# Kernel tuning notes

Hardware: AMD Instinct MI355X
Metric: run time of the kernel (lower is better)

## Reference

```python
import jax, jax.numpy as jnp
import numpy as np

SIGMA = 0.002  # TreeEnergyLoss default; edge weight = exp(-||df||^2 / sigma)


def bilinear_resize(x, oh, ow):
    """F.interpolate(mode='bilinear', align_corners=False), no antialias. x: [B,C,H,W]."""
    B, C, H, W = x.shape
    if (H, W) == (oh, ow):
        return x
    def coords(o, n):
        s = (jnp.arange(o, dtype=jnp.float32) + 0.5) * (n / o) - 0.5
        s = jnp.clip(s, 0.0, n - 1.0)
        lo = jnp.floor(s).astype(jnp.int32)
        hi = jnp.minimum(lo + 1, n - 1)
        return lo, hi, s - lo.astype(jnp.float32)
    r0, r1, rf = coords(oh, H)
    c0, c1, cf = coords(ow, W)
    xr = x[:, :, r0, :] * (1.0 - rf)[None, None, :, None] + x[:, :, r1, :] * rf[None, None, :, None]
    return xr[:, :, :, c0] * (1.0 - cf) + xr[:, :, :, c1] * cf


def nearest_resize(x, oh, ow):
    B, C, H, W = x.shape
    if (H, W) == (oh, ow):
        return x
    ri = jnp.floor(jnp.arange(oh) * (H / oh)).astype(jnp.int32)
    ci = jnp.floor(jnp.arange(ow) * (W / ow)).astype(jnp.int32)
    return x[:, :, ri, :][:, :, :, ci]


def _mst_bfs_np(embed, H, W):
    """Kruskal MST on the 4-connected pixel grid (edge cost = squared L2 feature
    distance, as in MinimumSpanningTree(TreeFilter2D.norm2_distance)), then BFS
    order from vertex 0. embed: np [C,H,W]. Returns (sorted_index, sorted_parent)
    where sorted_parent is the BFS position of each vertex's parent."""
    V = H * W
    idx = np.arange(V).reshape(H, W)
    eu = np.concatenate([idx[:-1, :].ravel(), idx[:, :-1].ravel()])
    ev = np.concatenate([idx[1:, :].ravel(), idx[:, 1:].ravel()])
    f = embed.reshape(embed.shape[0], V)
    cost = ((f[:, eu] - f[:, ev]) ** 2).sum(0)
    parent = np.arange(V)
    def find(x):
        root = x
        while parent[root] != root:
            root = parent[root]
        while parent[x] != root:
            parent[x], x = root, parent[x]
        return root
    nbr = [[] for _ in range(V)]
    cnt = 0
    for e in np.argsort(cost, kind='stable'):
        u, v = int(eu[e]), int(ev[e])
        ru, rv = find(u), find(v)
        if ru != rv:
            parent[ru] = rv
            nbr[u].append(v)
            nbr[v].append(u)
            cnt += 1
            if cnt == V - 1:
                break
    sorted_index = np.empty(V, np.int32)
    sorted_parent = np.empty(V, np.int32)
    visited = np.zeros(V, bool)
    sorted_index[0] = 0; sorted_parent[0] = 0; visited[0] = True
    head, tail = 0, 1
    while head < tail:
        u = int(sorted_index[head])
        for v in nbr[u]:
            if not visited[v]:
                visited[v] = True
                sorted_index[tail] = v
                sorted_parent[tail] = head
                tail += 1
        head += 1
    return sorted_index, sorted_parent


def build_trees(embed):
    """embed: [B,C,H,W]. Host-side MST+BFS per batch element (torch.no_grad in original)."""
    e = np.asarray(jax.lax.stop_gradient(embed), dtype=np.float64)
    B, C, H, W = e.shape
    si, sp = zip(*[_mst_bfs_np(e[b], H, W) for b in range(B)])
    return jnp.asarray(np.stack(si)), jnp.asarray(np.stack(sp))


def _tree_filter_single(f, embed, sorted_index, sorted_parent):
    """Normalized tree filter: out_i = sum_j W_ij f_j / sum_j W_ij with
    W_ij = prod of exp(-||de||^2/sigma) along the unique tree path i->j.
    Computed exactly via bottom-up aggregation + top-down propagation in BFS order.
    f: [C,V], embed: [Ce,V]."""
    C, V = f.shape
    fs = f[:, sorted_index]                        # [C,V] features in BFS order
    es = embed[:, sorted_index]
    d = ((es - es[:, sorted_parent]) ** 2).sum(0)  # [V]; d[0]=0 (root self edge)
    w = jnp.exp(-d / SIGMA)                        # edge weight to parent
    # bottom-up: children have larger BFS index, so reverse order is valid.
    # extra ones-row carries the normalizer Z through the same recursion.
    S0 = jnp.concatenate([fs, jnp.ones((1, V), fs.dtype)], axis=0)
    def up(S, j):
        return S.at[:, sorted_parent[j]].add(w[j] * S[:, j]), None
    S, _ = jax.lax.scan(up, S0, jnp.arange(V - 1, 0, -1))
    # top-down: A_root = S_root; A_j = S_j + w_j * (A_parent - w_j * S_j)
    def down(A, j):
        p = sorted_parent[j]
        return A.at[:, j].set(S[:, j] + w[j] * (A[:, p] - w[j] * S[:, j])), None
    A0 = jnp.zeros_like(S).at[:, 0].set(S[:, 0])
    A, _ = jax.lax.scan(down, A0, jnp.arange(1, V))
    out_sorted = A[:C] / A[C]
    return jnp.zeros_like(f).at[:, sorted_index].set(out_sorted)


def tree_filter(feature, embed, si, sp):
    B, C, h, w = feature.shape
    out = jax.vmap(_tree_filter_single)(
        feature.reshape(B, C, h * w),
        embed.reshape(B, embed.shape[1], h * w), si, sp)
    return out.reshape(B, C, h, w)


def setup_inputs():
    key = jax.random.key(0)
    k1, k2, k3, k4 = jax.random.split(key, 4)
    preds = jax.random.normal(k1, (8, 21, 80, 80), jnp.float32)
    # scaled so exp(-||df||^2 / 0.002) gives non-degenerate edge weights
    low_feats = jax.random.uniform(k2, (8, 3, 80, 80), jnp.float32) * 0.02
    high_feats = jax.random.normal(k3, (8, 256, 80, 80), jnp.float32) * 0.002
    unlabeled_ROIs = jax.random.randint(k4, (8, 80, 80), 0, 2, dtype=jnp.int32)
    return {"preds": preds, "low_feats": low_feats,
            "high_feats": high_feats, "unlabeled_ROIs": unlabeled_ROIs}


def reference(preds, low_feats, high_feats, unlabeled_ROIs):
    B, C, h, w = preds.shape
    low = bilinear_resize(low_feats, h, w)  # under torch.no_grad in original
    roi = nearest_resize(unlabeled_ROIs[:, None].astype(jnp.float32), h, w)
    si_l, sp_l = build_trees(low)
    si_h, sp_h = build_trees(high_feats)
    prob = jax.nn.softmax(preds, axis=1)
    AS = tree_filter(prob, jax.lax.stop_gradient(low), si_l, sp_l)  # low-level tree
    AS = tree_filter(AS, high_feats, si_h, sp_h)                    # high-level tree
    N = roi.sum()
    loss = (roi * jnp.abs(prob - AS)).sum()
    return jnp.where(N > 0, loss / N, jnp.zeros((), preds.dtype))  # weight = 1.0
```

## Files before the change

### kernel.cpp

```cpp
#include <hip/hip_runtime.h>

#define BB 8
#define CP 21
#define CF 22
#define CLOW 3
#define CHIGH 256
#define WW 80
#define VV 6400
#define EVERT 6320
#define EE 12640
#define TT 16
#define SIGMA_F 0.002f
#define ROOT 3240

#define NE (VV - 1)
#define NA (2 * NE)
#define NILA 0xFFFFu
#define NB 200

__device__ __forceinline__ void edge_uv(int e, int& u, int& v) {
  if (e < EVERT) { u = e; v = e + WW; }
  else { int e2 = e - EVERT; int r = e2 / (WW - 1); int c = e2 - r * (WW - 1); u = r * WW + c; v = u + 1; }
}

__global__ void k_softmax(const float* __restrict__ preds, float* __restrict__ prob) {
  int i = blockIdx.x * blockDim.x + threadIdx.x;
  if (i >= BB * VV) return;
  int b = i / VV, v = i - b * VV;
  const float* p = preds + (size_t)b * CP * VV + v;
  float m = -1e30f;
  #pragma unroll
  for (int c = 0; c < CP; c++) m = fmaxf(m, p[c * VV]);
  float e[CP], s = 0.f;
  #pragma unroll
  for (int c = 0; c < CP; c++) { float x = expf(p[c * VV] - m); e[c] = x; s += x; }
  float inv = 1.f / s;
  float* o = prob + (size_t)b * CP * VV + v;
  #pragma unroll
  for (int c = 0; c < CP; c++) o[c * VV] = e[c] * inv;
}

__global__ void k_edgekey(const float* __restrict__ low, const float* __restrict__ high,
                          unsigned long long* __restrict__ ekey) {
  int i = blockIdx.x * blockDim.x + threadIdx.x;
  if (i >= TT * EE) return;
  int t = i / EE, e = i - t * EE;
  int u, v; edge_uv(e, u, v);
  double acc = 0.0;
  if (t < BB) {
    const float* emb = low + (size_t)t * CLOW * VV;
    for (int c = 0; c < CLOW; c++) { double d = (double)emb[c * VV + u] - (double)emb[c * VV + v]; acc += d * d; }
  } else {
    const float* emb = high + (size_t)(t - BB) * CHIGH * VV;
    for (int c = 0; c < CHIGH; c++) { double d = (double)emb[c * VV + u] - (double)emb[c * VV + v]; acc += d * d; }
  }
  unsigned long long bits = (unsigned long long)__double_as_longlong(acc);
  ekey[i] = (bits & ~0x3FFFULL) | (unsigned long long)e;
}

__global__ __launch_bounds__(1024) void k_boruvka(const unsigned long long* __restrict__ ekey,
    int* __restrict__ mstU, int* __restrict__ mstV) {
  int t = blockIdx.x;
  const unsigned long long* key = ekey + (size_t)t * EE;
  int* mu = mstU + t * VV;
  int* mv = mstV + t * VV;
  __shared__ int comp[VV];
  __shared__ unsigned long long bst[VV];
  __shared__ unsigned short tgtS[VV];
  __shared__ unsigned short el0[EE];
  __shared__ unsigned short el1[EE];
  __shared__ int changed, cnt, necnt;
  int tid = threadIdx.x;
  const int nt = 1024;
  for (int v = tid; v < VV; v += nt) comp[v] = v;
  for (int e = tid; e < EE; e += nt) el0[e] = (unsigned short)e;
  if (tid == 0) cnt = 0;
  __syncthreads();
  unsigned short* els = el0;
  unsigned short* eld = el1;
  int ecnt = EE;
  for (int round = 0; round < 48 && ecnt > 0; round++) {
    for (int v = tid; v < VV; v += nt) bst[v] = ~0ULL;
    if (tid == 0) { changed = 0; necnt = 0; }
    __syncthreads();
    for (int j = tid; j < ecnt; j += nt) {
      int e = els[j];
      int u, v; edge_uv(e, u, v);
      int cu = comp[u], cv = comp[v];
      if (cu != cv) { unsigned long long k = key[e]; atomicMin(&bst[cu], k); atomicMin(&bst[cv], k); }
    }
    __syncthreads();
    for (int c = tid; c < VV; c += nt) {
      unsigned short tg = (unsigned short)NILA;
      if (comp[c] == c) {
        unsigned long long k = bst[c];
        if (k != ~0ULL) {
          int e = (int)(k & 0x3FFFULL);
          int u, v; edge_uv(e, u, v);
          int cu = comp[u], cv = comp[v];
          tg = (unsigned short)((cu == c) ? cv : cu);
        }
      }
      tgtS[c] = tg;
    }
    __syncthreads();
    for (int c = tid; c < VV; c += nt) {
      int o = tgtS[c];
      if (o == (int)NILA) continue;
      unsigned long long k = bst[c];
      if (bst[o] == k && c < o) continue;
      comp[c] = o;
      int slot = atomicAdd(&cnt, 1);
      int e = (int)(k & 0x3FFFULL);
      int u, v; edge_uv(e, u, v);
      mu[slot] = u; mv[slot] = v;
      changed = 1;
    }
    __syncthreads();
    if (!changed) break;
    for (int v = tid; v < VV; v += nt) {
      int c = comp[v];
      int c2 = comp[c];
      if (c2 != c) {
        int r0 = c2;
        while (true) { int n = comp[r0]; if (n == r0) break; r0 = n; }
        comp[v] = r0;
      }
    }
    __syncthreads();
    for (int j = tid; j < ecnt; j += nt) {
      int e = els[j];
      int u, v; edge_uv(e, u, v);
      if (comp[u] != comp[v]) { int s = atomicAdd(&necnt, 1); eld[s] = (unsigned short)e; }
    }
    __syncthreads();
    ecnt = necnt;
    __syncthreads();
    unsigned short* tp = els; els = eld; eld = tp;
  }
}

__global__ __launch_bounds__(1024) void k_buildtree(const int* __restrict__ mstU, const int* __restrict__ mstV,
    int* __restrict__ ordG, int* __restrict__ spG, int* __restrict__ pvG,
    int* __restrict__ lpG, int* __restrict__ nlevG) {
  int t = blockIdx.x;
  const int* mu = mstU + t * VV;
  const int* mv = mstV + t * VV;
  int tid = threadIdx.x;
  const int nt = 1024;
  int lane = tid & 63, wid = tid >> 6;

  __shared__ int buf4[32004];
  char* buf = (char*)buf4;
  __shared__ int part[64];
  __shared__ short tbl[8 * NB];
  __shared__ unsigned short dbuf2[VV];
  __shared__ int lasts, spackU, spackW, scenter, smaxd;

  int* deg = (int*)(buf + 0);
  int* off = (int*)(buf + 25600);
  unsigned short* adjA = (unsigned short*)(buf + 51208);
  unsigned short* succ = (unsigned short*)(buf + 102408);
  int* pk0 = (int*)(buf + 0);
  int* pk1 = (int*)(buf + 51208);
  unsigned short* r_a = (unsigned short*)(buf + 102408);
  short* H = (short*)(buf + 51208);
  unsigned short* depthR = (unsigned short*)(buf + 76808);
  unsigned short* firstK = (unsigned short*)(buf + 89608);
  short* prefmin = (short*)(buf + 0);
  short* sufmin  = (short*)(buf + 25600);
  unsigned short* distU = (unsigned short*)(buf + 76808);
  unsigned short* parentS = (unsigned short*)(buf + 76808);
  int* lev = (int*)(buf + 0);
  int* cur = (int*)(buf + 25604);
  unsigned short* ordS = (unsigned short*)(buf + 51208);
  unsigned short* posS = (unsigned short*)(buf + 64008);

  auto blockScanEx = [&](int s) -> int {
    int x = s;
    #pragma unroll
    for (int d = 1; d < 64; d <<= 1) { int o = __shfl_up(x, d); if (lane >= d) x += o; }
    if (lane == 63) part[wid] = x;
    __syncthreads();
    if (wid == 0) {
      int y = (lane < 16) ? part[lane] : 0;
      #pragma unroll
      for (int d = 1; d < 16; d <<= 1) { int o = __shfl_up(y, d); if (lane >= d) y += o; }
      if (lane < 16) part[lane] = y;
    }
    __syncthreads();
    int base = (wid > 0) ? part[wid - 1] : 0;
    return base + (x - s);
  };

  for (int v = tid; v < VV; v += nt) deg[v] = 0;
  __syncthreads();
  for (int e = tid; e < NE; e += nt) { atomicAdd(&deg[mu[e]], 1); atomicAdd(&deg[mv[e]], 1); }
  __syncthreads();
  {
    const int SCH = 7;
    int base = tid * SCH;
    int s = 0;
    #pragma unroll
    for (int k = 0; k < SCH; k++) { int v = base + k; if (v < VV) s += deg[v]; }
    int ex = blockScanEx(s);
    #pragma unroll
    for (int k = 0; k < SCH; k++) { int v = base + k; if (v < VV) { off[v] = ex; ex += deg[v]; } }
    if (tid == 1023) off[VV] = ex;
  }
  __syncthreads();
  for (int v = tid; v < VV; v += nt) deg[v] = off[v];
  __syncthreads();
  for (int e = tid; e < NE; e += nt) {
    int u = mu[e], v = mv[e];
    adjA[atomicAdd(&deg[u], 1)] = (unsigned short)(2 * e);
    adjA[atomicAdd(&deg[v], 1)] = (unsigned short)(2 * e + 1);
  }
  __syncthreads();
  for (int v = tid; v < VV; v += nt) {
    int b0 = off[v], dv = off[v + 1] - b0;
    for (int k = 0; k < dv; k++) {
      unsigned short a = adjA[b0 + k];
      unsigned short b = adjA[b0 + ((k + 1 == dv) ? 0 : k + 1)];
      succ[a ^ 1] = b;
    }
  }
  if (tid == 0) lasts = adjA[off[ROOT] + (off[ROOT + 1] - off[ROOT]) - 1] ^ 1;
  __syncthreads();
  if (tid == 0) succ[lasts] = (unsigned short)NILA;
  __syncthreads();
  for (int a = tid; a < NA; a += nt) {
    unsigned int n = succ[a];
    pk0[a] = ((n == NILA ? 0 : 1) << 16) | (int)n;
  }
  __syncthreads();
  {
    int* px = pk0;
    int* py = pk1;
    for (int rd = 0; rd < 14; rd++) {
      for (int a = tid; a < NA; a += nt) {
        int cur_ = px[a];
        int n = cur_ & 0xFFFF;
        if (n != (int)NILA) {
          int o = px[n];
          cur_ = (((cur_ >> 16) + (o >> 16)) << 16) | (o & 0xFFFF);
        }
        py[a] = cur_;
      }
      __syncthreads();
      int* tp = px; px = py; py = tp;
    }
    for (int a = tid; a < NA; a += nt) r_a[a] = (unsigned short)(pk0[a] >> 16);
  }
  __syncthreads();
  for (int a = tid; a < NA; a += nt) {
    int pa = NA - 1 - (int)r_a[a];
    int pb = NA - 1 - (int)r_a[a ^ 1];
    H[pa] = (pa < pb) ? (short)1 : (short)-1;
  }
  __syncthreads();
  {
    const int SCH = 13;
    int base = tid * SCH;
    int lim = base + SCH; if (lim > NA) lim = NA;
    int s = 0;
    for (int j = base; j < lim; j++) s += H[j];
    int run = blockScanEx(s);
    for (int j = base; j < lim; j++) { run += H[j]; H[j] = (short)run; }
  }
  __syncthreads();
  if (tid == 0) { spackU = 0; smaxd = 0; scenter = 0x7FFFFFFF; }
  __syncthreads();
  for (int a = tid; a < NA; a += nt) {
    int pa = NA - 1 - (int)r_a[a];
    int pb = NA - 1 - (int)r_a[a ^ 1];
    if (pa < pb) {
      int e = a >> 1;
      int head = (a & 1) ? mu[e] : mv[e];
      depthR[head] = (unsigned short)H[pa];
      firstK[head] = (unsigned short)(pa + 1);
    }
  }
  if (tid == 0) { depthR[ROOT] = 0; firstK[ROOT] = 0; }
  __syncthreads();
  {
    int loc = 0;
    for (int v = tid; v < VV; v += nt) { int p = ((int)depthR[v] << 13) | v; if (p > loc) loc = p; }
    #pragma unroll
    for (int d = 32; d > 0; d >>= 1) { int o = __shfl_down(loc, d); if (o > loc) loc = o; }
    if (lane == 0) atomicMax(&spackU, loc);
  }
  __syncthreads();
  {
    for (int seg = wid; seg < NB; seg += 16) {
      int p = seg * 64 + lane;
      int h = (p < NA) ? (int)H[p] : 32767;
      int hp = h;
      #pragma unroll
      for (int d = 1; d < 64; d <<= 1) { int o = __shfl_up(hp, d); if (lane >= d && o < hp) hp = o; }
      prefmin[p] = (short)hp;
      int hs = h;
      #pragma unroll
      for (int d = 1; d < 64; d <<= 1) { int o = __shfl_down(hs, d); if (lane + d < 64 && o < hs) hs = o; }
      sufmin[p] = (short)hs;
      if (lane == 0) tbl[seg] = (short)hs;
    }
  }
  __syncthreads();
  for (int k = 1; k < 8; k++) {
    short vv_ = 0;
    if (tid < NB) {
      int o = tid + (1 << (k - 1));
      short a = tbl[(k - 1) * NB + tid];
      short b2 = (o < NB) ? tbl[(k - 1) * NB + o] : (short)32767;
      vv_ = (a < b2) ? a : b2;
    }
    __syncthreads();
    if (tid < NB) tbl[k * NB + tid] = vv_;
    __syncthreads();
  }
  auto distq = [&](int K1, int K2) -> int {
    if (K1 == K2) return 0;
    int l = (K1 < K2 ? K1 : K2) - 1;
    int r = (K1 > K2 ? K1 : K2) - 1;
    int m = 32767;
    int l0 = l < 0 ? 0 : l;
    int bl = l0 >> 6, br = r >> 6;
    if (bl == br) {
      for (int p = l0; p <= r; p++) { int h = H[p]; if (h < m) m = h; }
    } else {
      int a = sufmin[l0], b2 = prefmin[r];
      m = a < b2 ? a : b2;
      int lo = bl + 1, hi = br - 1;
      if (lo <= hi) {
        int L = hi - lo + 1;
        int k = 31 - __builtin_clz(L);
        int c1 = tbl[k * NB + lo];
        int c2 = tbl[k * NB + hi - (1 << k) + 1];
        if (c1 < m) m = c1;
        if (c2 < m) m = c2;
      }
    }
    if (l < 0 && 0 < m) m = 0;
    int h1 = (K1 == 0) ? 0 : (int)H[K1 - 1];
    int h2 = (K2 == 0) ? 0 : (int)H[K2 - 1];
    return h1 + h2 - 2 * m;
  };
  int u = spackU & 0x1FFF;
  int Ku = firstK[u];
  if (tid == 0) spackW = 0;
  __syncthreads();
  {
    int loc = 0;
    for (int v = tid; v < VV; v += nt) {
      int d = distq(Ku, firstK[v]);
      distU[v] = (unsigned short)d;
      int p = (d << 13) | v;
      if (p > loc) loc = p;
    }
    #pragma unroll
    for (int d = 32; d > 0; d >>= 1) { int o = __shfl_down(loc, d); if (o > loc) loc = o; }
    if (lane == 0) atomicMax(&spackW, loc);
  }
  __syncthreads();
  int D = spackW >> 13;
  int w = spackW & 0x1FFF;
  int Kw = firstK[w];
  for (int v = tid; v < VV; v += nt) dbuf2[v] = (unsigned short)distq(Kw, firstK[v]);
  __syncthreads();
  {
    int half = D >> 1;
    for (int v = tid; v < VV; v += nt) {
      if ((int)distU[v] == half && (int)distU[v] + (int)dbuf2[v] == D) atomicMin(&scenter, v);
    }
  }
  __syncthreads();
  int cvert = (scenter == 0x7FFFFFFF) ? ROOT : scenter;
  int Kc = firstK[cvert];
  __syncthreads();
  {
    int loc = 0;
    for (int v = tid; v < VV; v += nt) {
      int d = distq(Kc, firstK[v]);
      dbuf2[v] = (unsigned short)d;
      if (d > loc) loc = d;
    }
    #pragma unroll
    for (int d = 32; d > 0; d >>= 1) { int o = __shfl_down(loc, d); if (o > loc) loc = o; }
    if (lane == 0) atomicMax(&smaxd, loc);
  }
  __syncthreads();
  int maxd = smaxd;
  int sTil = Kc;
  for (int a = tid; a < NA; a += nt) {
    int pa = NA - 1 - (int)r_a[a];
    int pb = NA - 1 - (int)r_a[a ^ 1];
    int pa2 = pa - sTil; if (pa2 < 0) pa2 += NA;
    int pb2 = pb - sTil; if (pb2 < 0) pb2 += NA;
    if (pa2 < pb2) {
      int e = a >> 1;
      int head = (a & 1) ? mu[e] : mv[e];
      int tail = (a & 1) ? mv[e] : mu[e];
      parentS[head] = (unsigned short)tail;
    }
  }
  if (tid == 0) parentS[cvert] = (unsigned short)cvert;
  __syncthreads();
  for (int d = tid; d <= VV; d += nt) lev[d] = 0;
  __syncthreads();
  for (int v = tid; v < VV; v += nt) atomicAdd(&lev[dbuf2[v]], 1);
  __syncthreads();
  {
    const int SCH = 7;
    int base = tid * SCH;
    int s = 0;
    #pragma unroll
    for (int k = 0; k < SCH; k++) { int d = base + k; if (d <= VV) s += lev[d]; }
    int ex = blockScanEx(s);
    #pragma unroll
    for (int k = 0; k < SCH; k++) {
      int d = base + k;
      if (d <= VV) {
        int st = ex;
        ex += lev[d];
        if (d < VV) cur[d] = st;
        lpG[t * (VV + 1) + d] = st;
      }
    }
  }
  __syncthreads();
  for (int v = tid; v < VV; v += nt) {
    int d = dbuf2[v];
    int slot = atomicAdd(&cur[d], 1);
    ordS[slot] = (unsigned short)v;
    posS[v] = (unsigned short)slot;
  }
  __syncthreads();
  for (int j = tid; j < VV; j += nt) {
    int v = ordS[j];
    int pv = parentS[v];
    ordG[t * VV + j] = v;
    pvG[t * VV + j] = pv;
    spG[t * VV + j] = posS[pv];
  }
  if (tid == 0) nlevG[t] = maxd + 1;
}

__global__ void k_weights(const unsigned long long* __restrict__ ekey,
                          const int* __restrict__ ordG, const int* __restrict__ pvG,
                          float* __restrict__ wvp) {
  int i = blockIdx.x * blockDim.x + threadIdx.x;
  if (i >= TT * VV) return;
  int t = i / VV;
  int v = ordG[i], p = pvG[i];
  float wout;
  if (v == p) {
    wout = 1.0f;
  } else {
    int a = v < p ? v : p;
    int diff = v < p ? p - v : v - p;
    int e;
    if (diff == WW) e = a;
    else { int r = a / WW, c = a - r * WW; e = EVERT + r * (WW - 1) + c; }
    unsigned long long k = ekey[(size_t)t * EE + e];
    double cost = __longlong_as_double((long long)(k & ~0x3FFFULL));
    wout = expf(-(float)cost / SIGMA_F);
  }
  wvp[i] = wout;
}

__global__ __launch_bounds__(512) void k_filter_pc(const float* __restrict__ Fsrc, float* __restrict__ Araw,
    const float* __restrict__ wvp, const int* __restrict__ ordG, const int* __restrict__ spG,
    const int* __restrict__ lpG, const int* __restrict__ nlevG, int treeBase) {
  int blk = blockIdx.x;
  int b = blk / CF, ch = blk - b * CF;
  int t = treeBase + b;
  __shared__ alignas(16) char arena[140816];
  float2* ab0 = (float2*)(arena);
  float2* ab1 = (float2*)(arena + 51200);
  float*  S   = (float*)(arena + 51200);
  float*  w   = (float*)(arena + 76800);
  unsigned short* sp0 = (unsigned short*)(arena + 102400);
  unsigned short* sp1 = (unsigned short*)(arena + 115200);
  unsigned short* lpS = (unsigned short*)(arena + 128000);
  const int* ord = ordG + t * VV;
  const int* spt = spG + t * VV;
  const float* wsrc = wvp + t * VV;
  const int* lp = lpG + t * (VV + 1);
  int tid = threadIdx.x;
  const int nt = 512;
  int NL = nlevG[t];
  for (int j = tid; j <= NL; j += nt) lpS[j] = (unsigned short)lp[j];
  const bool norm_in = (treeBase != 0);
  for (int j = tid; j < VV; j += nt) {
    sp0[j] = (unsigned short)spt[j];
    w[j] = wsrc[j];
    float val;
    if (ch < CP) {
      int v = ord[j];
      if (!norm_in) val = Fsrc[((size_t)b * CP + ch) * VV + v];
      else          val = Fsrc[((size_t)b * CF + ch) * VV + v] / Fsrc[((size_t)b * CF + CP) * VV + v];
    } else val = 1.0f;
    S[j] = val;
  }
  __syncthreads();
  if (tid < 64) {
    int s1 = lpS[NL];
    int s0 = lpS[NL - 1];
    for (int l = NL - 1; l >= 1; l--) {
      int s0n = (l > 1) ? (int)lpS[l - 1] : 0;
      for (int j = s0 + tid; j < s1; j += 64) {
        atomicAdd(&S[sp0[j]], w[j] * S[j]);
      }
      asm volatile("s_waitcnt lgkmcnt(0)" ::: "memory");
      __builtin_amdgcn_sched_barrier(0);
      s1 = s0; s0 = s0n;
    }
  }
  __syncthreads();
  for (int j = tid; j < VV; j += nt) {
    float wv = w[j];
    float a = (j == 0) ? 0.f : wv;
    float bv = (j == 0) ? S[0] : S[j] * (1.f - wv * wv);
    ab0[j] = make_float2(a, bv);
  }
  __syncthreads();
  int rounds = 0;
  { int d = 1; while (d < NL) { d <<= 1; rounds++; } }
  float2 *abs_ = ab0, *abd_ = ab1;
  unsigned short *ps_ = sp0, *pd_ = sp1;
  for (int r = 0; r < rounds; r++) {
    for (int j = tid; j < VV; j += nt) {
      float2 m = abs_[j];
      int p = ps_[j];
      float2 o = m;
      int pn = p;
      if (m.x != 0.f) {
        float2 mp = abs_[p];
        pn = ps_[p];
        o.x = m.x * mp.x;
        o.y = fmaf(m.x, mp.y, m.y);
      }
      abd_[j] = o;
      pd_[j] = (unsigned short)pn;
    }
    __syncthreads();
    float2* tf = abs_; abs_ = abd_; abd_ = tf;
    unsigned short* tu = ps_; ps_ = pd_; pd_ = tu;
  }
  float* Ob = Araw + ((size_t)b * CF + ch) * VV;
  for (int j = tid; j < VV; j += nt) Ob[ord[j]] = abs_[j].y;
}

__global__ void k_loss(const float* __restrict__ prob, const float* __restrict__ Araw2,
                       const int* __restrict__ roi, double* __restrict__ acc) {
  int i = blockIdx.x * blockDim.x + threadIdx.x;
  int tid = threadIdx.x;
  double s = 0.0, n = 0.0;
  if (i < BB * VV) {
    int b = i / VV, v = i - b * VV;
    if (roi[i] != 0) {
      n = 1.0;
      const float* pb = prob + (size_t)b * CP * VV + v;
      const float* ab = Araw2 + (size_t)b * CF * VV + v;
      float inv = 1.0f / ab[CP * VV];
      float ls = 0.f;
      #pragma unroll
      for (int c = 0; c < CP; c++) ls += fabsf(pb[c * VV] - ab[c * VV] * inv);
      s = (double)ls;
    }
  }
  __shared__ double rs[256], rn[256];
  rs[tid] = s; rn[tid] = n;
  __syncthreads();
  for (int d = 128; d > 0; d >>= 1) {
    if (tid < d) { rs[tid] += rs[tid + d]; rn[tid] += rn[tid + d]; }
    __syncthreads();
  }
  if (tid == 0) { atomicAdd(&acc[0], rs[0]); atomicAdd(&acc[1], rn[0]); }
}

__global__ void k_finalize(const double* __restrict__ acc, float* __restrict__ out) {
  out[0] = (acc[1] > 0.0) ? (float)(acc[0] / acc[1]) : 0.0f;
}

extern "C" void kernel_launch(void* const* d_in, const int* in_sizes, int n_in,
                              void* d_out, int out_size, void* d_ws, size_t ws_size,
                              hipStream_t stream) {
  const float* preds = (const float*)d_in[0];
  const float* low   = (const float*)d_in[1];
  const float* high  = (const float*)d_in[2];
  const int*   roi   = (const int*)d_in[3];
  float* out = (float*)d_out;

  char* w = (char*)d_ws;
  size_t off = 0;
  auto alloc = [&](size_t bytes) -> void* {
    void* p = w + off;
    off += (bytes + 255) & ~(size_t)255;
    return p;
  };
  float* prob  = (float*)alloc((size_t)BB * CP * VV * 4);
  float* Araw1 = (float*)alloc((size_t)BB * CF * VV * 4);
  float* Araw2 = (float*)alloc((size_t)BB * CF * VV * 4);
  unsigned long long* ekey = (unsigned long long*)alloc((size_t)TT * EE * 8);
  int* mstU = (int*)alloc((size_t)TT * VV * 4);
  int* mstV = (int*)alloc((size_t)TT * VV * 4);
  int* ordG = (int*)alloc((size_t)TT * VV * 4);
  int* spG  = (int*)alloc((size_t)TT * VV * 4);
  int* pvG  = (int*)alloc((size_t)TT * VV * 4);
  int* lpG  = (int*)alloc((size_t)TT * (VV + 1) * 4);
  int* nlev = (int*)alloc((size_t)TT * 4);
  float* wvp = (float*)alloc((size_t)TT * VV * 4);
  double* acc = (double*)alloc(16);

  hipMemsetAsync(acc, 0, 16, stream);

  k_softmax<<<(BB * VV + 255) / 256, 256, 0, stream>>>(preds, prob);
  k_edgekey<<<(TT * EE + 255) / 256, 256, 0, stream>>>(low, high, ekey);
  k_boruvka<<<TT, 1024, 0, stream>>>(ekey, mstU, mstV);
  k_buildtree<<<TT, 1024, 0, stream>>>(mstU, mstV, ordG, spG, pvG, lpG, nlev);
  k_weights<<<(TT * VV + 255) / 256, 256, 0, stream>>>(ekey, ordG, pvG, wvp);
  k_filter_pc<<<BB * CF, 512, 0, stream>>>(prob,  Araw1, wvp, ordG, spG, lpG, nlev, 0);
  k_filter_pc<<<BB * CF, 512, 0, stream>>>(Araw1, Araw2, wvp, ordG, spG, lpG, nlev, BB);
  k_loss<<<(BB * VV + 255) / 256, 256, 0, stream>>>(prob, Araw2, roi, acc);
  k_finalize<<<1, 1, 0, stream>>>(acc, out);
}
```

Baseline: 300.1 us.

## Replace level-serial tree sweeps and pointer-jumping with 4-level ancestor-jump sweeps

The tree filter's upward aggregation and downward propagation are restructured. Two block-parallel doubling steps build grandparent and great-grandparent pointers with combined weights. This lets the single-wavefront serial sweep step four BFS levels per iteration instead of one, and it replaces the log-round pointer-jumping scan in the downward pass with a second 4-level serial sweep. The root weight is now zero, so root-edge terms vanish and zero contributions are skipped. This trades the per-level wavefront waits and the scan rounds for several extra block-wide passes and barriers, plus more shared memory.

```diff
diff --git a/kernel.cpp b/kernel.cpp
--- a/kernel.cpp
+++ b/kernel.cpp
@@ -17,6 +17,7 @@
 #define NA (2 * NE)
 #define NILA 0xFFFFu
 #define NB 200
+#define FCH 13
 
 __device__ __forceinline__ void edge_uv(int e, int& u, int& v) {
   if (e < EVERT) { u = e; v = e + WW; }
@@ -455,7 +456,7 @@
   int v = ordG[i], p = pvG[i];
   float wout;
   if (v == p) {
-    wout = 1.0f;
+    wout = 0.0f;
   } else {
     int a = v < p ? v : p;
     int diff = v < p ? p - v : v - p;
@@ -475,14 +476,15 @@
   int blk = blockIdx.x;
   int b = blk / CF, ch = blk - b * CF;
   int t = treeBase + b;
-  __shared__ alignas(16) char arena[140816];
-  float2* ab0 = (float2*)(arena);
-  float2* ab1 = (float2*)(arena + 51200);
-  float*  S   = (float*)(arena + 51200);
-  float*  w   = (float*)(arena + 76800);
-  unsigned short* sp0 = (unsigned short*)(arena + 102400);
-  unsigned short* sp1 = (unsigned short*)(arena + 115200);
-  unsigned short* lpS = (unsigned short*)(arena + 128000);
+  __shared__ alignas(16) char arena[153664];
+  float* w    = (float*)(arena);
+  unsigned short* sp0 = (unsigned short*)(arena + 25600);
+  float* s    = (float*)(arena + 38400);
+  unsigned short* anc2 = (unsigned short*)(arena + 64000);
+  float* w2   = (float*)(arena + 76800);
+  float* t_   = (float*)(arena + 102400);
+  unsigned short* anc4 = (unsigned short*)(arena + 128000);
+  unsigned short* lpS  = (unsigned short*)(arena + 140800);
   const int* ord = ordG + t * VV;
   const int* spt = spG + t * VV;
   const float* wsrc = wvp + t * VV;
@@ -492,64 +494,118 @@
   int NL = nlevG[t];
   for (int j = tid; j <= NL; j += nt) lpS[j] = (unsigned short)lp[j];
   const bool norm_in = (treeBase != 0);
-  for (int j = tid; j < VV; j += nt) {
-    sp0[j] = (unsigned short)spt[j];
-    w[j] = wsrc[j];
-    float val;
-    if (ch < CP) {
-      int v = ord[j];
-      if (!norm_in) val = Fsrc[((size_t)b * CP + ch) * VV + v];
-      else          val = Fsrc[((size_t)b * CF + ch) * VV + v] / Fsrc[((size_t)b * CF + CP) * VV + v];
-    } else val = 1.0f;
-    S[j] = val;
-  }
-  __syncthreads();
+  #pragma unroll
+  for (int k = 0; k < FCH; k++) {
+    int j = tid + k * nt;
+    if (j < VV) {
+      sp0[j] = (unsigned short)spt[j];
+      w[j] = (j == 0) ? 0.f : wsrc[j];
+      float val;
+      if (ch < CP) {
+        int v = ord[j];
+        if (!norm_in) val = Fsrc[((size_t)b * CP + ch) * VV + v];
+        else          val = Fsrc[((size_t)b * CF + ch) * VV + v] / Fsrc[((size_t)b * CF + CP) * VV + v];
+      } else val = 1.0f;
+      s[j] = val;
+    }
+  }
+  __syncthreads();
+  #pragma unroll
+  for (int k = 0; k < FCH; k++) {
+    int j = tid + k * nt;
+    if (j < VV) { int p = sp0[j]; anc2[j] = sp0[p]; w2[j] = w[j] * w[p]; }
+  }
+  __syncthreads();
+  #pragma unroll
+  for (int k = 0; k < FCH; k++) { int j = tid + k * nt; if (j < VV) t_[j] = s[j]; }
+  __syncthreads();
+  #pragma unroll
+  for (int k = 0; k < FCH; k++) {
+    int j = tid + k * nt;
+    if (j < VV) { float c = w[j] * s[j]; if (c != 0.f) atomicAdd(&t_[sp0[j]], c); }
+  }
+  __syncthreads();
+  #pragma unroll
+  for (int k = 0; k < FCH; k++) { int j = tid + k * nt; if (j < VV) s[j] = t_[j]; }
+  __syncthreads();
+  #pragma unroll
+  for (int k = 0; k < FCH; k++) {
+    int j = tid + k * nt;
+    if (j < VV) { float c = w2[j] * t_[j]; if (c != 0.f) atomicAdd(&s[anc2[j]], c); }
+  }
+  __syncthreads();
+  {
+    float rw[FCH];
+    #pragma unroll
+    for (int k = 0; k < FCH; k++) {
+      int j = tid + k * nt;
+      if (j < VV) { int p2 = anc2[j]; rw[k] = w2[j] * w2[p2]; anc4[j] = anc2[p2]; }
+    }
+    __syncthreads();
+    #pragma unroll
+    for (int k = 0; k < FCH; k++) { int j = tid + k * nt; if (j < VV) w2[j] = rw[k]; }
+  }
+  __syncthreads();
+  int G = (NL + 3) >> 2;
   if (tid < 64) {
-    int s1 = lpS[NL];
-    int s0 = lpS[NL - 1];
-    for (int l = NL - 1; l >= 1; l--) {
-      int s0n = (l > 1) ? (int)lpS[l - 1] : 0;
-      for (int j = s0 + tid; j < s1; j += 64) {
-        atomicAdd(&S[sp0[j]], w[j] * S[j]);
+    for (int g = G - 2; g >= 0; g--) {
+      int lo = lpS[4 * g + 4];
+      int hl = 4 * g + 8; if (hl > NL) hl = NL;
+      int hi = lpS[hl];
+      for (int j = lo + tid; j < hi; j += 64) {
+        float c = w2[j] * s[j];
+        if (c != 0.f) atomicAdd(&s[anc4[j]], c);
       }
       asm volatile("s_waitcnt lgkmcnt(0)" ::: "memory");
       __builtin_amdgcn_sched_barrier(0);
-      s1 = s0; s0 = s0n;
-    }
-  }
-  __syncthreads();
-  for (int j = tid; j < VV; j += nt) {
-    float wv = w[j];
-    float a = (j == 0) ? 0.f : wv;
-    float bv = (j == 0) ? S[0] : S[j] * (1.f - wv * wv);
-    ab0[j] = make_float2(a, bv);
-  }
-  __syncthreads();
-  int rounds = 0;
-  { int d = 1; while (d < NL) { d <<= 1; rounds++; } }
-  float2 *abs_ = ab0, *abd_ = ab1;
-  unsigned short *ps_ = sp0, *pd_ = sp1;
-  for (int r = 0; r < rounds; r++) {
-    for (int j = tid; j < VV; j += nt) {
-      float2 m = abs_[j];
-      int p = ps_[j];
-      float2 o = m;
-      int pn = p;
-      if (m.x != 0.f) {
-        float2 mp = abs_[p];
-        pn = ps_[p];
-        o.x = m.x * mp.x;
-        o.y = fmaf(m.x, mp.y, m.y);
+    }
+  }
+  __syncthreads();
+  #pragma unroll
+  for (int k = 0; k < FCH; k++) {
+    int j = tid + k * nt;
+    if (j < VV) { float wv = w[j]; s[j] *= (1.f - wv * wv); }
+  }
+  __syncthreads();
+  #pragma unroll
+  for (int k = 0; k < FCH; k++) {
+    int j = tid + k * nt;
+    if (j < VV) {
+      int p = sp0[j];
+      float av = w[j];
+      w2[j] = av * w[p];
+      t_[j] = fmaf(av, s[p], s[j]);
+    }
+  }
+  __syncthreads();
+  #pragma unroll
+  for (int k = 0; k < FCH; k++) {
+    int j = tid + k * nt;
+    if (j < VV) {
+      int p2 = anc2[j];
+      float av = w2[j];
+      w[j] = av * w2[p2];
+      s[j] = fmaf(av, t_[p2], t_[j]);
+    }
+  }
+  __syncthreads();
+  if (tid < 64) {
+    for (int g = 1; g < G; g++) {
+      int lo = lpS[4 * g];
+      int hl = 4 * g + 4; if (hl > NL) hl = NL;
+      int hi = lpS[hl];
+      for (int j = lo + tid; j < hi; j += 64) {
+        float av = w[j];
+        if (av != 0.f) s[j] = fmaf(av, s[anc4[j]], s[j]);
       }
-      abd_[j] = o;
-      pd_[j] = (unsigned short)pn;
-    }
-    __syncthreads();
-    float2* tf = abs_; abs_ = abd_; abd_ = tf;
-    unsigned short* tu = ps_; ps_ = pd_; pd_ = tu;
-  }
+      asm volatile("s_waitcnt lgkmcnt(0)" ::: "memory");
+      __builtin_amdgcn_sched_barrier(0);
+    }
+  }
+  __syncthreads();
   float* Ob = Araw + ((size_t)b * CF + ch) * VV;
-  for (int j = tid; j < VV; j += nt) Ob[ord[j]] = abs_[j].y;
+  #pragma unroll
+  for (int k = 0; k < FCH; k++) { int j = tid + k * nt; if (j < VV) Ob[ord[j]] = s[j]; }
 }
 
 __global__ void k_loss(const float* __restrict__ prob, const float* __restrict__ Araw2,
```

New measurement: 335.4 us. 1.12x slower.

## Order BFS children contiguously; replace atomic upsweep and pointer-jumping with level sweeps

Applied to the files above, without the earlier changes.

The tree build now places each vertex's children in consecutive slots within the next BFS level and emits a packed child-count/first-child table. The filter's upward pass gathers children directly instead of issuing LDS atomicAdds. The downward pass becomes a sequential per-level sweep instead of log-depth pointer-jumping rounds over all vertices. This cuts LDS footprint and per-round full-array passes, but the downward sweep now runs on a single wavefront across all levels, which may serialize deep trees.

```diff
diff --git a/kernel.cpp b/kernel.cpp
--- a/kernel.cpp
+++ b/kernel.cpp
@@ -142,7 +142,7 @@
 
 __global__ __launch_bounds__(1024) void k_buildtree(const int* __restrict__ mstU, const int* __restrict__ mstV,
     int* __restrict__ ordG, int* __restrict__ spG, int* __restrict__ pvG,
-    int* __restrict__ lpG, int* __restrict__ nlevG) {
+    int* __restrict__ lpG, unsigned short* __restrict__ csG, int* __restrict__ nlevG) {
   int t = blockIdx.x;
   const int* mu = mstU + t * VV;
   const int* mv = mstV + t * VV;
@@ -171,10 +171,12 @@
   short* sufmin  = (short*)(buf + 25600);
   unsigned short* distU = (unsigned short*)(buf + 76808);
   unsigned short* parentS = (unsigned short*)(buf + 76808);
-  int* lev = (int*)(buf + 0);
-  int* cur = (int*)(buf + 25604);
-  unsigned short* ordS = (unsigned short*)(buf + 51208);
-  unsigned short* posS = (unsigned short*)(buf + 64008);
+  int* lvA = (int*)(buf + 0);
+  int* curB = (int*)(buf + 25604);
+  int* cntC = (int*)(buf + 51208);
+  unsigned short* spanS = (unsigned short*)(buf + 89608);
+  unsigned short* ordS = (unsigned short*)(buf + 102408);
+  unsigned short* posS = (unsigned short*)(buf + 115208);
 
   auto blockScanEx = [&](int s) -> int {
     int x = s;
@@ -406,35 +408,49 @@
   }
   if (tid == 0) parentS[cvert] = (unsigned short)cvert;
   __syncthreads();
-  for (int d = tid; d <= VV; d += nt) lev[d] = 0;
-  __syncthreads();
-  for (int v = tid; v < VV; v += nt) atomicAdd(&lev[dbuf2[v]], 1);
+  for (int d = tid; d <= VV; d += nt) lvA[d] = 0;
+  for (int v = tid; v < VV; v += nt) cntC[v] = 0;
+  __syncthreads();
+  for (int v = tid; v < VV; v += nt) {
+    atomicAdd(&lvA[dbuf2[v]], 1);
+    if (v != cvert) atomicAdd(&cntC[parentS[v]], 1);
+  }
   __syncthreads();
   {
     const int SCH = 7;
     int base = tid * SCH;
     int s = 0;
     #pragma unroll
-    for (int k = 0; k < SCH; k++) { int d = base + k; if (d <= VV) s += lev[d]; }
+    for (int k = 0; k < SCH; k++) { int d = base + k; if (d <= VV) s += lvA[d]; }
     int ex = blockScanEx(s);
     #pragma unroll
     for (int k = 0; k < SCH; k++) {
       int d = base + k;
       if (d <= VV) {
         int st = ex;
-        ex += lev[d];
-        if (d < VV) cur[d] = st;
+        ex += lvA[d];
+        if (d < VV) curB[d] = st;
         lpG[t * (VV + 1) + d] = st;
       }
     }
   }
   __syncthreads();
   for (int v = tid; v < VV; v += nt) {
-    int d = dbuf2[v];
-    int slot = atomicAdd(&cur[d], 1);
-    ordS[slot] = (unsigned short)v;
-    posS[v] = (unsigned short)slot;
-  }
+    int cc = cntC[v];
+    if (cc > 0) spanS[v] = (unsigned short)atomicAdd(&curB[(int)dbuf2[v] + 1], cc);
+  }
+  __syncthreads();
+  for (int v = tid; v < VV; v += nt) lvA[v] = 0;
+  __syncthreads();
+  for (int v = tid; v < VV; v += nt) {
+    if (v != cvert) {
+      int p = parentS[v];
+      int pos = spanS[p] + atomicAdd(&lvA[p], 1);
+      posS[v] = (unsigned short)pos;
+      ordS[pos] = (unsigned short)v;
+    }
+  }
+  if (tid == 0) { posS[cvert] = 0; ordS[0] = (unsigned short)cvert; }
   __syncthreads();
   for (int j = tid; j < VV; j += nt) {
     int v = ordS[j];
@@ -442,6 +458,8 @@
     ordG[t * VV + j] = v;
     pvG[t * VV + j] = pv;
     spG[t * VV + j] = posS[pv];
+    int cc = cntC[v];
+    csG[t * VV + j] = (unsigned short)((cc << 13) | (cc ? (int)spanS[v] : 0));
   }
   if (tid == 0) nlevG[t] = maxd + 1;
 }
@@ -455,7 +473,7 @@
   int v = ordG[i], p = pvG[i];
   float wout;
   if (v == p) {
-    wout = 1.0f;
+    wout = 0.0f;
   } else {
     int a = v < p ? v : p;
     int diff = v < p ? p - v : v - p;
@@ -471,20 +489,20 @@
 
 __global__ __launch_bounds__(512) void k_filter_pc(const float* __restrict__ Fsrc, float* __restrict__ Araw,
     const float* __restrict__ wvp, const int* __restrict__ ordG, const int* __restrict__ spG,
+    const unsigned short* __restrict__ csG,
     const int* __restrict__ lpG, const int* __restrict__ nlevG, int treeBase) {
   int blk = blockIdx.x;
   int b = blk / CF, ch = blk - b * CF;
   int t = treeBase + b;
-  __shared__ alignas(16) char arena[140816];
-  float2* ab0 = (float2*)(arena);
-  float2* ab1 = (float2*)(arena + 51200);
-  float*  S   = (float*)(arena + 51200);
-  float*  w   = (float*)(arena + 76800);
-  unsigned short* sp0 = (unsigned short*)(arena + 102400);
-  unsigned short* sp1 = (unsigned short*)(arena + 115200);
-  unsigned short* lpS = (unsigned short*)(arena + 128000);
+  __shared__ alignas(16) char arena[89608];
+  float* w   = (float*)(arena);
+  float* s   = (float*)(arena + 25600);
+  unsigned short* sp0  = (unsigned short*)(arena + 51200);
+  unsigned short* cspk = (unsigned short*)(arena + 64000);
+  unsigned short* lpS  = (unsigned short*)(arena + 76800);
   const int* ord = ordG + t * VV;
   const int* spt = spG + t * VV;
+  const unsigned short* cst = csG + (size_t)t * VV;
   const float* wsrc = wvp + t * VV;
   const int* lp = lpG + t * (VV + 1);
   int tid = threadIdx.x;
@@ -494,6 +512,7 @@
   const bool norm_in = (treeBase != 0);
   for (int j = tid; j < VV; j += nt) {
     sp0[j] = (unsigned short)spt[j];
+    cspk[j] = cst[j];
     w[j] = wsrc[j];
     float val;
     if (ch < CP) {
@@ -501,55 +520,43 @@
       if (!norm_in) val = Fsrc[((size_t)b * CP + ch) * VV + v];
       else          val = Fsrc[((size_t)b * CF + ch) * VV + v] / Fsrc[((size_t)b * CF + CP) * VV + v];
     } else val = 1.0f;
-    S[j] = val;
+    s[j] = val;
   }
   __syncthreads();
   if (tid < 64) {
-    int s1 = lpS[NL];
-    int s0 = lpS[NL - 1];
-    for (int l = NL - 1; l >= 1; l--) {
-      int s0n = (l > 1) ? (int)lpS[l - 1] : 0;
+    for (int l = NL - 2; l >= 0; l--) {
+      int s0 = lpS[l], s1 = lpS[l + 1];
       for (int j = s0 + tid; j < s1; j += 64) {
-        atomicAdd(&S[sp0[j]], w[j] * S[j]);
+        unsigned short pk = cspk[j];
+        int cn = pk >> 13;
+        int c0 = pk & 0x1FFF;
+        float acc = s[j];
+        for (int k = 0; k < cn; k++) acc += w[c0 + k] * s[c0 + k];
+        s[j] = acc;
       }
       asm volatile("s_waitcnt lgkmcnt(0)" ::: "memory");
       __builtin_amdgcn_sched_barrier(0);
-      s1 = s0; s0 = s0n;
     }
   }
   __syncthreads();
   for (int j = tid; j < VV; j += nt) {
     float wv = w[j];
-    float a = (j == 0) ? 0.f : wv;
-    float bv = (j == 0) ? S[0] : S[j] * (1.f - wv * wv);
-    ab0[j] = make_float2(a, bv);
-  }
-  __syncthreads();
-  int rounds = 0;
-  { int d = 1; while (d < NL) { d <<= 1; rounds++; } }
-  float2 *abs_ = ab0, *abd_ = ab1;
-  unsigned short *ps_ = sp0, *pd_ = sp1;
-  for (int r = 0; r < rounds; r++) {
-    for (int j = tid; j < VV; j += nt) {
-      float2 m = abs_[j];
-      int p = ps_[j];
-      float2 o = m;
-      int pn = p;
-      if (m.x != 0.f) {
-        float2 mp = abs_[p];
-        pn = ps_[p];
-        o.x = m.x * mp.x;
-        o.y = fmaf(m.x, mp.y, m.y);
+    s[j] *= (1.f - wv * wv);
+  }
+  __syncthreads();
+  if (tid < 64) {
+    for (int l = 1; l < NL; l++) {
+      int s0 = lpS[l], s1 = lpS[l + 1];
+      for (int j = s0 + tid; j < s1; j += 64) {
+        s[j] = fmaf(w[j], s[sp0[j]], s[j]);
       }
-      abd_[j] = o;
-      pd_[j] = (unsigned short)pn;
-    }
-    __syncthreads();
-    float2* tf = abs_; abs_ = abd_; abd_ = tf;
-    unsigned short* tu = ps_; ps_ = pd_; pd_ = tu;
-  }
+      asm volatile("s_waitcnt lgkmcnt(0)" ::: "memory");
+      __builtin_amdgcn_sched_barrier(0);
+    }
+  }
+  __syncthreads();
   float* Ob = Araw + ((size_t)b * CF + ch) * VV;
-  for (int j = tid; j < VV; j += nt) Ob[ord[j]] = abs_[j].y;
+  for (int j = tid; j < VV; j += nt) Ob[ord[j]] = s[j];
 }
 
 __global__ void k_loss(const float* __restrict__ prob, const float* __restrict__ Araw2,
@@ -610,6 +617,7 @@
   int* spG  = (int*)alloc((size_t)TT * VV * 4);
   int* pvG  = (int*)alloc((size_t)TT * VV * 4);
   int* lpG  = (int*)alloc((size_t)TT * (VV + 1) * 4);
+  unsigned short* csG = (unsigned short*)alloc((size_t)TT * VV * 2);
   int* nlev = (int*)alloc((size_t)TT * 4);
   float* wvp = (float*)alloc((size_t)TT * VV * 4);
   double* acc = (double*)alloc(16);
@@ -619,10 +627,10 @@
   k_softmax<<<(BB * VV + 255) / 256, 256, 0, stream>>>(preds, prob);
   k_edgekey<<<(TT * EE + 255) / 256, 256, 0, stream>>>(low, high, ekey);
   k_boruvka<<<TT, 1024, 0, stream>>>(ekey, mstU, mstV);
-  k_buildtree<<<TT, 1024, 0, stream>>>(mstU, mstV, ordG, spG, pvG, lpG, nlev);
+  k_buildtree<<<TT, 1024, 0, stream>>>(mstU, mstV, ordG, spG, pvG, lpG, csG, nlev);
   k_weights<<<(TT * VV + 255) / 256, 256, 0, stream>>>(ekey, ordG, pvG, wvp);
-  k_filter_pc<<<BB * CF, 512, 0, stream>>>(prob,  Araw1, wvp, ordG, spG, lpG, nlev, 0);
-  k_filter_pc<<<BB * CF, 512, 0, stream>>>(Araw1, Araw2, wvp, ordG, spG, lpG, nlev, BB);
+  k_filter_pc<<<BB * CF, 512, 0, stream>>>(prob,  Araw1, wvp, ordG, spG, csG, lpG, nlev, 0);
+  k_filter_pc<<<BB * CF, 512, 0, stream>>>(Araw1, Araw2, wvp, ordG, spG, csG, lpG, nlev, BB);
   k_loss<<<(BB * VV + 255) / 256, 256, 0, stream>>>(prob, Araw2, roi, acc);
   k_finalize<<<1, 1, 0, stream>>>(acc, out);
 }
```

After: 419.9 us. +39.9%, slower.
